# Kernel optimization log

Hardware: AMD Instinct MI355X
Metric: run time of the kernel (lower is better)

## Reference

```python
import jax, jax.numpy as jnp
import numpy as np

B, C, H, W = 8, 2, 512, 512  # features hard-coded to 2 by Conv3x3(2,1)
N_ATTN = 6  # 3 ResidualAttentionUnits x 2 AttentionConv each
HALF = C // 2


def _conv1x1(x, w, b):
    # x: [B,C,H,W], w: [O,C], b: [O]
    return jnp.einsum('bchw,oc->bohw', x, w) + b[None, :, None, None]


def _unfold3(x):
    # x: [B,C,H+2,W+2] -> [B,C,H,W,3,3] (height-window, width-window), matching
    # torch unfold(2,3,1).unfold(3,3,1)
    Hh = x.shape[2] - 2
    Ww = x.shape[3] - 2
    return jnp.stack(
        [jnp.stack([x[:, :, i:i + Hh, j:j + Ww] for j in range(3)], axis=-1)
         for i in range(3)], axis=-2)


def _attn_conv(x, wq, bq, wk, bk, wv, bv, rh, rw):
    # Local 3x3 window self-attention (AttentionConv, groups=1).
    b_, c_, h_, w_ = x.shape
    xp = jnp.pad(x, ((0, 0), (0, 0), (1, 1), (1, 1)))  # zero pad=1
    q = _conv1x1(x, wq, bq)                 # [B,Co,H,W]
    k = _unfold3(_conv1x1(xp, wk, bk))      # [B,Co,H,W,3,3]
    v = _unfold3(_conv1x1(xp, wv, bv))
    co = q.shape[1]
    half = co // 2
    # rh, rw: [half,3]; rel_h broadcast over kh, rel_w over kw
    k = jnp.concatenate([
        k[:, :half] + rh[None, :, None, None, :, None],
        k[:, half:] + rw[None, :, None, None, None, :]], axis=1)
    k = k.reshape(b_, co, h_, w_, 9)
    v = v.reshape(b_, co, h_, w_, 9)
    attn = jax.nn.softmax(q[..., None] * k, axis=-1)  # softmax over 9 window positions
    return jnp.einsum('bchwk,bchwk->bchw', attn, v)


def _rau(x, p, u):
    # ResidualAttentionUnit: relu -> atten1 -> relu -> atten2 -> +x
    wq, bq, wk, bk, wv, bv, rh, rw = p
    i, j = 2 * u, 2 * u + 1
    h = jax.nn.relu(x)
    h = _attn_conv(h, wq[i], bq[i], wk[i], bk[i], wv[i], bv[i], rh[i], rw[i])
    h = jax.nn.relu(h)
    h = _attn_conv(h, wq[j], bq[j], wk[j], bk[j], wv[j], bv[j], rh[j], rw[j])
    return h + x


def _up2_bilinear_ac(x):
    # bilinear, scale_factor=2, align_corners=True
    b_, c_, h_, w_ = x.shape
    ho, wo = 2 * h_, 2 * w_
    ys = jnp.linspace(0.0, h_ - 1.0, ho)
    xs = jnp.linspace(0.0, w_ - 1.0, wo)
    y0 = jnp.floor(ys).astype(jnp.int32)
    x0 = jnp.floor(xs).astype(jnp.int32)
    y1 = jnp.clip(y0 + 1, 0, h_ - 1)
    x1 = jnp.clip(x0 + 1, 0, w_ - 1)
    wy = (ys - y0)[None, None, :, None]
    wx = (xs - x0)[None, None, None, :]
    r0 = x[:, :, y0, :]
    r1 = x[:, :, y1, :]
    v00 = r0[:, :, :, x0]
    v01 = r0[:, :, :, x1]
    v10 = r1[:, :, :, x0]
    v11 = r1[:, :, :, x1]
    return (v00 * (1 - wy) * (1 - wx) + v01 * (1 - wy) * wx
            + v10 * wy * (1 - wx) + v11 * wy * wx)


def _forward(input_1, input_2, wq, bq, wk, bk, wv, bv, rh, rw, conv_w, conv_b):
    p = (wq, bq, wk, bk, wv, bv, rh, rw)
    out = _rau(input_1, p, 0) + _rau(input_2, p, 1)
    out = _rau(out, p, 2)
    xp = jnp.pad(out, ((0, 0), (0, 0), (1, 1), (1, 1)), mode='reflect')
    out = jax.lax.conv_general_dilated(
        xp, conv_w, (1, 1), 'VALID',
        dimension_numbers=('NCHW', 'OIHW', 'NCHW')) + conv_b[None, :, None, None]
    out = jax.nn.sigmoid(out)
    return out, _up2_bilinear_ac(out)


def setup_inputs() -> dict:
    key = jax.random.key(0)
    ks = jax.random.split(key, 12)
    return {
        'input_1': jax.random.normal(ks[0], (B, C, H, W), jnp.float32),
        'input_2': jax.random.normal(ks[1], (B, C, H, W), jnp.float32),
        # stacked params for the 6 AttentionConv modules (all bias=True)
        'wq': jax.random.normal(ks[2], (N_ATTN, C, C), jnp.float32) * 0.5,
        'bq': jax.random.normal(ks[3], (N_ATTN, C), jnp.float32) * 0.1,
        'wk': jax.random.normal(ks[4], (N_ATTN, C, C), jnp.float32) * 0.5,
        'bk': jax.random.normal(ks[5], (N_ATTN, C), jnp.float32) * 0.1,
        'wv': jax.random.normal(ks[6], (N_ATTN, C, C), jnp.float32) * 0.5,
        'bv': jax.random.normal(ks[7], (N_ATTN, C), jnp.float32) * 0.1,
        'rh': jax.random.normal(ks[8], (N_ATTN, HALF, 3), jnp.float32),
        'rw': jax.random.normal(ks[9], (N_ATTN, HALF, 3), jnp.float32),
        # Conv3x3(2,1): reflection-pad + 3x3 conv
        'conv_w': jax.random.normal(ks[10], (1, 2, 3, 3), jnp.float32) * 0.2,
        'conv_b': jax.random.normal(ks[11], (1,), jnp.float32) * 0.1,
    }


def reference(input_1, input_2, wq, bq, wk, bk, wv, bv, rh, rw, conv_w, conv_b):
    return _forward(input_1, input_2, wq, bq, wk, bk, wv, bv, rh, rw, conv_w, conv_b)
```

## Files before the change

### kernel.cpp

```cpp
#include <hip/hip_runtime.h>

#if __has_builtin(__builtin_amdgcn_exp2f)
#define EXP2F(x) __builtin_amdgcn_exp2f(x)
#else
#define EXP2F(x) exp2f(x)
#endif

typedef float v2f __attribute__((ext_vector_type(2)));

constexpr int B = 8, H = 512, W = 512;
constexpr int PLANE = H * W;
constexpr int BSTRIDE = 2 * PLANE;
constexpr int NPIX = B * PLANE;
constexpr int UPN = B * 1024 * 1024;
constexpr int PPITCH = 520;
constexpr int PXOFF  = 4;
constexpr int PPLANE = H * PPITCH;
constexpr int PBUF   = 16 * PPLANE;
constexpr float LOG2E = 1.4426950408889634f;

__device__ __forceinline__ float reluf(float v) { return v > 0.f ? v : 0.f; }
__device__ __forceinline__ float frcp(float v) { return __builtin_amdgcn_rcpf(v); }
__device__ __forceinline__ v2f vfma(v2f a, v2f b, v2f c) { return __builtin_elementwise_fma(a, b, c); }
__device__ __forceinline__ v2f vmax2(v2f a, v2f b) { return __builtin_elementwise_max(a, b); }
__device__ __forceinline__ v2f bc(float x) { v2f r; r.x = x; r.y = x; return r; }

struct AttnW {
    v2f wq0, wq1, bq;
    v2f wk0, wk1;
    v2f biasK[3];
    float rwL[3];
    v2f wv0, wv1, bv;
};

__device__ __forceinline__ AttnW load_w(
    const float* wq, const float* bq, const float* wk, const float* bk,
    const float* wv, const float* bv, const float* rh, const float* rw, int i)
{
    AttnW P;
    P.wq0.x = wq[4*i];   P.wq0.y = wq[4*i+2];
    P.wq1.x = wq[4*i+1]; P.wq1.y = wq[4*i+3];
    P.bq.x  = bq[2*i];   P.bq.y  = bq[2*i+1];
    P.wk0.x = wk[4*i]   * LOG2E; P.wk0.y = wk[4*i+2] * LOG2E;
    P.wk1.x = wk[4*i+1] * LOG2E; P.wk1.y = wk[4*i+3] * LOG2E;
    float bk1L = bk[2*i+1] * LOG2E;
#pragma unroll
    for (int r = 0; r < 3; ++r) {
        P.biasK[r].x = (bk[2*i] + rh[3*i+r]) * LOG2E;
        P.biasK[r].y = bk1L;
    }
#pragma unroll
    for (int d = 0; d < 3; ++d) P.rwL[d] = rw[3*i+d] * LOG2E;
    P.wv0.x = wv[4*i];   P.wv0.y = wv[4*i+2];
    P.wv1.x = wv[4*i+1]; P.wv1.y = wv[4*i+3];
    P.bv.x  = bv[2*i];   P.bv.y  = bv[2*i+1];
    return P;
}

__device__ __forceinline__ void attn_strip(
    const v2f (&t)[3][6], const AttnW& P, v2f (&o)[4])
{
    v2f kk[3][6], vv[3][6];
#pragma unroll
    for (int r = 0; r < 3; ++r)
#pragma unroll
        for (int c = 0; c < 6; ++c) {
            v2f u0 = bc(t[r][c].x), u1 = bc(t[r][c].y);
            kk[r][c] = vfma(P.wk0, u0, vfma(P.wk1, u1, P.biasK[r]));
            vv[r][c] = vfma(P.wv0, u0, vfma(P.wv1, u1, P.bv));
        }
#pragma unroll
    for (int px = 0; px < 4; ++px) {
        v2f q = vfma(P.wq0, bc(t[1][px+1].x), vfma(P.wq1, bc(t[1][px+1].y), P.bq));
        v2f addv[3];
#pragma unroll
        for (int d = 0; d < 3; ++d) { addv[d].x = 0.f; addv[d].y = q.y * P.rwL[d]; }
        v2f s[9];
#pragma unroll
        for (int r = 0; r < 3; ++r)
#pragma unroll
            for (int d = 0; d < 3; ++d)
                s[r*3+d] = vfma(q, kk[r][px+d], addv[d]);
        v2f m = vmax2(vmax2(vmax2(vmax2(s[0], s[1]), vmax2(s[2], s[3])),
                            vmax2(vmax2(s[4], s[5]), vmax2(s[6], s[7]))), s[8]);
        v2f sum = bc(0.f), acc = bc(0.f);
#pragma unroll
        for (int r = 0; r < 3; ++r)
#pragma unroll
            for (int d = 0; d < 3; ++d) {
                v2f dd = s[r*3+d] - m;
                v2f e; e.x = EXP2F(dd.x); e.y = EXP2F(dd.y);
                sum += e;
                acc = vfma(e, vv[r][px+d], acc);
            }
        v2f rs; rs.x = frcp(sum.x); rs.y = frcp(sum.y);
        o[px] = acc * rs;
    }
}

__device__ __forceinline__ void write_pads(float* outp, int b2, int y, int x0)
{
    float4 z = make_float4(0.f, 0.f, 0.f, 0.f);
    if (x0 == 0) {
        int pb = b2 * PPLANE + y * PPITCH;
        *reinterpret_cast<float4*>(outp + pb)          = z;
        *reinterpret_cast<float4*>(outp + pb + PPLANE) = z;
    } else if (x0 == W - 4) {
        int pb = b2 * PPLANE + y * PPITCH + PXOFF + W;
        *reinterpret_cast<float4*>(outp + pb)          = z;
        *reinterpret_cast<float4*>(outp + pb + PPLANE) = z;
    }
}

__global__ __launch_bounds__(256) void attn_in_kernel(
    const float* __restrict__ xA, const float* __restrict__ xB,
    float* __restrict__ outA, float* __restrict__ outB,
    const float* __restrict__ wq, const float* __restrict__ bq,
    const float* __restrict__ wk, const float* __restrict__ bk,
    const float* __restrict__ wv, const float* __restrict__ bv,
    const float* __restrict__ rh, const float* __restrict__ rw,
    int piA, int piB)
{
    int bid = blockIdx.x;
    bool second = bid >= 2048;
    const float* x = second ? xB : xA;
    float* outp = second ? outB : outA;
    int pi = second ? piB : piA;

    int s  = (second ? bid - 2048 : bid) * 256 + threadIdx.x;
    int x0 = (s & 127) * 4;
    int y  = (s >> 7) & 511;
    int b  = s >> 16;

    AttnW P = load_w(wq, bq, wk, bk, wv, bv, rh, rw, pi);

    const float* xb = x + b * BSTRIDE;
    bool rowv[3] = { y > 0, true, y < H - 1 };
    int  yr[3]   = { y > 0 ? y - 1 : 0, y, y < H - 1 ? y + 1 : H - 1 };
    bool lv   = x0 > 0;
    bool rvld = x0 < W - 4;
    int  xl = lv ? x0 - 1 : 0;
    int  xr = rvld ? x0 + 4 : W - 1;

    v2f t[3][6];
#pragma unroll
    for (int r = 0; r < 3; ++r) {
        const float* p0 = xb + yr[r] * W;
        const float* p1 = p0 + PLANE;
        float4 a0 = *reinterpret_cast<const float4*>(p0 + x0);
        float4 a1 = *reinterpret_cast<const float4*>(p1 + x0);
        float u0[6] = { p0[xl], a0.x, a0.y, a0.z, a0.w, p0[xr] };
        float u1[6] = { p1[xl], a1.x, a1.y, a1.z, a1.w, p1[xr] };
        bool rv_ = rowv[r];
#pragma unroll
        for (int c = 0; c < 6; ++c) {
            bool ok = rv_ && (c > 0 || lv) && (c < 5 || rvld);
            t[r][c].x = ok ? reluf(u0[c]) : 0.f;
            t[r][c].y = ok ? reluf(u1[c]) : 0.f;
        }
    }

    v2f o[4];
    attn_strip(t, P, o);

    int ob = (b * 2) * PPLANE + y * PPITCH + x0 + PXOFF;
    *reinterpret_cast<float4*>(outp + ob)          = make_float4(o[0].x, o[1].x, o[2].x, o[3].x);
    *reinterpret_cast<float4*>(outp + ob + PPLANE) = make_float4(o[0].y, o[1].y, o[2].y, o[3].y);
    write_pads(outp, b * 2, y, x0);
}

template<int NRES, bool PADOUT>
__global__ __launch_bounds__(256) void attn_fast_kernel(
    const float* __restrict__ xp,
    float* __restrict__ outp, int oPlane, int oPitch, int oXoff,
    const float* __restrict__ res0, int aPlane, int aPitch, int aXoff,
    const float* __restrict__ res1, int cPlane, int cPitch, int cXoff,
    const float* __restrict__ wq, const float* __restrict__ bq,
    const float* __restrict__ wk, const float* __restrict__ bk,
    const float* __restrict__ wv, const float* __restrict__ bv,
    const float* __restrict__ rh, const float* __restrict__ rw, int pi)
{
    int s  = blockIdx.x * 256 + threadIdx.x;
    int x0 = (s & 127) * 4;
    int y  = (s >> 7) & 511;
    int b  = s >> 16;

    AttnW P = load_w(wq, bq, wk, bk, wv, bv, rh, rw, pi);

    const float* xb0 = xp + (b * 2) * PPLANE + x0 + PXOFF;
    v2f t[3][6];
#pragma unroll
    for (int r = 0; r < 3; ++r) {
        int gy = y - 1 + r;
        bool ok = (unsigned)gy < (unsigned)H;
        int gyc = ok ? gy : y;
        const float* p0 = xb0 + gyc * PPITCH;
        const float* p1 = p0 + PPLANE;
        float4 a0 = *reinterpret_cast<const float4*>(p0);
        float4 a1 = *reinterpret_cast<const float4*>(p1);
        float e0l = p0[-1], e0r = p0[4];
        float e1l = p1[-1], e1r = p1[4];
        if (ok) {
            t[r][0].x=reluf(e0l);  t[r][0].y=reluf(e1l);
            t[r][1].x=reluf(a0.x); t[r][1].y=reluf(a1.x);
            t[r][2].x=reluf(a0.y); t[r][2].y=reluf(a1.y);
            t[r][3].x=reluf(a0.z); t[r][3].y=reluf(a1.z);
            t[r][4].x=reluf(a0.w); t[r][4].y=reluf(a1.w);
            t[r][5].x=reluf(e0r);  t[r][5].y=reluf(e1r);
        } else {
#pragma unroll
            for (int c = 0; c < 6; ++c) { t[r][c].x = 0.f; t[r][c].y = 0.f; }
        }
    }

    v2f o[4];
    attn_strip(t, P, o);

    if (NRES >= 1) {
        int rb = (b * 2) * aPlane + y * aPitch + x0 + aXoff;
        float4 ra = *reinterpret_cast<const float4*>(res0 + rb);
        float4 rbv = *reinterpret_cast<const float4*>(res0 + rb + aPlane);
        o[0].x+=ra.x; o[1].x+=ra.y; o[2].x+=ra.z; o[3].x+=ra.w;
        o[0].y+=rbv.x; o[1].y+=rbv.y; o[2].y+=rbv.z; o[3].y+=rbv.w;
    }
    if (NRES >= 2) {
        int rb = (b * 2) * cPlane + y * cPitch + x0 + cXoff;
        float4 ra = *reinterpret_cast<const float4*>(res1 + rb);
        float4 rbv = *reinterpret_cast<const float4*>(res1 + rb + cPlane);
        o[0].x+=ra.x; o[1].x+=ra.y; o[2].x+=ra.z; o[3].x+=ra.w;
        o[0].y+=rbv.x; o[1].y+=rbv.y; o[2].y+=rbv.z; o[3].y+=rbv.w;
    }

    int ob = (b * 2) * oPlane + y * oPitch + x0 + oXoff;
    *reinterpret_cast<float4*>(outp + ob)          = make_float4(o[0].x, o[1].x, o[2].x, o[3].x);
    *reinterpret_cast<float4*>(outp + ob + oPlane) = make_float4(o[0].y, o[1].y, o[2].y, o[3].y);
    if (PADOUT) write_pads(outp, b * 2, y, x0);
}

__global__ __launch_bounds__(256) void conv_sig4_kernel(
    const float* __restrict__ u,
    const float* __restrict__ cw, const float* __restrict__ cb,
    float* __restrict__ o)
{
    int s  = blockIdx.x * 256 + threadIdx.x;
    int x0 = (s & 127) * 4;
    int y  = (s >> 7) & 511;
    int b  = s >> 16;

    float w[18];
#pragma unroll
    for (int i = 0; i < 18; ++i) w[i] = cw[i];

    int yy[3];
#pragma unroll
    for (int i = 0; i < 3; ++i) {
        int t = y + i - 1;
        if (t < 0) t = -t;
        if (t > H - 1) t = 2 * (H - 1) - t;
        yy[i] = t;
    }
    int xl = x0 - 1; if (xl < 0) xl = 1;
    int xr = x0 + 4; if (xr > W - 1) xr = 2 * (W - 1) - xr;

    float acc[4] = { cb[0], cb[0], cb[0], cb[0] };
#pragma unroll
    for (int c = 0; c < 2; ++c) {
        const float* up = u + b * BSTRIDE + c * PLANE;
#pragma unroll
        for (int i = 0; i < 3; ++i) {
            const float* row = up + yy[i] * W;
            float4 a = *reinterpret_cast<const float4*>(row + x0);
            float t[6] = { row[xl], a.x, a.y, a.z, a.w, row[xr] };
#pragma unroll
            for (int j = 0; j < 3; ++j) {
                float wc = w[c * 9 + i * 3 + j];
#pragma unroll
                for (int px = 0; px < 4; ++px)
                    acc[px] = fmaf(t[px + j], wc, acc[px]);
            }
        }
    }
    float4 ov;
    ov.x = frcp(1.f + EXP2F(-acc[0] * LOG2E));
    ov.y = frcp(1.f + EXP2F(-acc[1] * LOG2E));
    ov.z = frcp(1.f + EXP2F(-acc[2] * LOG2E));
    ov.w = frcp(1.f + EXP2F(-acc[3] * LOG2E));
    *reinterpret_cast<float4*>(o + b * PLANE + y * W + x0) = ov;
}

__global__ __launch_bounds__(256) void upsample4_kernel(
    const float* __restrict__ o, float* __restrict__ up)
{
    int p  = blockIdx.x * 256 + threadIdx.x;
    int b  = p >> 18;
    int y  = (p >> 8) & 1023;
    int x0 = (p & 255) * 4;

    const float scale = 511.0f / 1023.0f;
    float fy = y * scale;
    int y0 = (int)fy;
    float wy = fy - y0;
    int y1 = min(y0 + 1, H - 1);

    const float* ob = o + b * PLANE;
    const float* row0 = ob + y0 * W;
    const float* row1 = ob + y1 * W;

    float4 ov;
    float* ovp = &ov.x;
#pragma unroll
    for (int j = 0; j < 4; ++j) {
        float fx = (x0 + j) * scale;
        int xi = (int)fx;
        float wx = fx - xi;
        int xi1 = min(xi + 1, W - 1);
        float v00 = row0[xi], v01 = row0[xi1];
        float v10 = row1[xi], v11 = row1[xi1];
        float top = fmaf(v01 - v00, wx, v00);
        float bot = fmaf(v11 - v10, wx, v10);
        ovp[j] = fmaf(bot - top, wy, top);
    }
    *reinterpret_cast<float4*>(up + ((long)b << 20) + y * 1024 + x0) = ov;
}

extern "C" void kernel_launch(void* const* d_in, const int* in_sizes, int n_in,
                              void* d_out, int out_size, void* d_ws, size_t ws_size,
                              hipStream_t stream) {
    const float* in1 = (const float*)d_in[0];
    const float* in2 = (const float*)d_in[1];
    const float* wq  = (const float*)d_in[2];
    const float* bq  = (const float*)d_in[3];
    const float* wk  = (const float*)d_in[4];
    const float* bk  = (const float*)d_in[5];
    const float* wv  = (const float*)d_in[6];
    const float* bv  = (const float*)d_in[7];
    const float* rh  = (const float*)d_in[8];
    const float* rw  = (const float*)d_in[9];
    const float* cw  = (const float*)d_in[10];
    const float* cb  = (const float*)d_in[11];

    float* out = (float*)d_out;
    float* A  = out;
    float* Bb = out + PBUF;
    float* C  = (float*)d_ws;
    (void)ws_size; (void)out_size; (void)n_in; (void)in_sizes;

    dim3 blk(256);

    attn_in_kernel<<<4096, blk, 0, stream>>>(in1, in2, A, Bb,
        wq, bq, wk, bk, wv, bv, rh, rw, 0, 2);
    attn_fast_kernel<1,false><<<2048, blk, 0, stream>>>(A, C, PLANE, W, 0,
        in1, PLANE, W, 0, nullptr, 0, 0, 0,
        wq, bq, wk, bk, wv, bv, rh, rw, 1);
    attn_fast_kernel<2,true><<<2048, blk, 0, stream>>>(Bb, A, PPLANE, PPITCH, PXOFF,
        in2, PLANE, W, 0, C, PLANE, W, 0,
        wq, bq, wk, bk, wv, bv, rh, rw, 3);
    attn_fast_kernel<0,true><<<2048, blk, 0, stream>>>(A, Bb, PPLANE, PPITCH, PXOFF,
        nullptr, 0, 0, 0, nullptr, 0, 0, 0,
        wq, bq, wk, bk, wv, bv, rh, rw, 4);
    attn_fast_kernel<1,false><<<2048, blk, 0, stream>>>(Bb, C, PLANE, W, 0,
        A, PPLANE, PPITCH, PXOFF, nullptr, 0, 0, 0,
        wq, bq, wk, bk, wv, bv, rh, rw, 5);
    conv_sig4_kernel<<<2048, blk, 0, stream>>>(C, cw, cb, out);
    upsample4_kernel<<<8192, blk, 0, stream>>>(out, out + NPIX);
}
```

Baseline: 115.7 us.

## Fuse all stages into one cooperative persistent kernel with grid barriers

```diff
diff --git a/kernel.cpp b/kernel.cpp
--- a/kernel.cpp
+++ b/kernel.cpp
@@ -12,7 +12,6 @@
 constexpr int PLANE = H * W;
 constexpr int BSTRIDE = 2 * PLANE;
 constexpr int NPIX = B * PLANE;
-constexpr int UPN = B * 1024 * 1024;
 constexpr int PPITCH = 520;
 constexpr int PXOFF  = 4;
 constexpr int PPLANE = H * PPITCH;
@@ -112,27 +111,13 @@
     }
 }
 
-__global__ __launch_bounds__(256) void attn_in_kernel(
-    const float* __restrict__ xA, const float* __restrict__ xB,
-    float* __restrict__ outA, float* __restrict__ outB,
-    const float* __restrict__ wq, const float* __restrict__ bq,
-    const float* __restrict__ wk, const float* __restrict__ bk,
-    const float* __restrict__ wv, const float* __restrict__ bv,
-    const float* __restrict__ rh, const float* __restrict__ rw,
-    int piA, int piB)
-{
-    int bid = blockIdx.x;
-    bool second = bid >= 2048;
-    const float* x = second ? xB : xA;
-    float* outp = second ? outB : outA;
-    int pi = second ? piB : piA;
-
-    int s  = (second ? bid - 2048 : bid) * 256 + threadIdx.x;
+
+__device__ __forceinline__ void attn_in_body(
+    unsigned s, const float* __restrict__ x, float* outp, const AttnW& P)
+{
     int x0 = (s & 127) * 4;
     int y  = (s >> 7) & 511;
     int b  = s >> 16;
-
-    AttnW P = load_w(wq, bq, wk, bk, wv, bv, rh, rw, pi);
 
     const float* xb = x + b * BSTRIDE;
     bool rowv[3] = { y > 0, true, y < H - 1 };
@@ -170,22 +155,16 @@
 }
 
 template<int NRES, bool PADOUT>
-__global__ __launch_bounds__(256) void attn_fast_kernel(
-    const float* __restrict__ xp,
-    float* __restrict__ outp, int oPlane, int oPitch, int oXoff,
-    const float* __restrict__ res0, int aPlane, int aPitch, int aXoff,
-    const float* __restrict__ res1, int cPlane, int cPitch, int cXoff,
-    const float* __restrict__ wq, const float* __restrict__ bq,
-    const float* __restrict__ wk, const float* __restrict__ bk,
-    const float* __restrict__ wv, const float* __restrict__ bv,
-    const float* __restrict__ rh, const float* __restrict__ rw, int pi)
-{
-    int s  = blockIdx.x * 256 + threadIdx.x;
+__device__ __forceinline__ void attn_fast_body(
+    unsigned s, const float* xp, float* outp,
+    int oPlane, int oPitch, int oXoff,
+    const float* res0, int aPlane, int aPitch, int aXoff,
+    const float* res1, int cPlane, int cPitch, int cXoff,
+    const AttnW& P)
+{
     int x0 = (s & 127) * 4;
     int y  = (s >> 7) & 511;
     int b  = s >> 16;
-
-    AttnW P = load_w(wq, bq, wk, bk, wv, bv, rh, rw, pi);
 
     const float* xb0 = xp + (b * 2) * PPLANE + x0 + PXOFF;
     v2f t[3][6];
@@ -237,19 +216,12 @@
     if (PADOUT) write_pads(outp, b * 2, y, x0);
 }
 
-__global__ __launch_bounds__(256) void conv_sig4_kernel(
-    const float* __restrict__ u,
-    const float* __restrict__ cw, const float* __restrict__ cb,
-    float* __restrict__ o)
-{
-    int s  = blockIdx.x * 256 + threadIdx.x;
+__device__ __forceinline__ void conv_body(
+    unsigned s, const float* u, const float (&w)[18], float cb0, float* o)
+{
     int x0 = (s & 127) * 4;
     int y  = (s >> 7) & 511;
     int b  = s >> 16;
-
-    float w[18];
-#pragma unroll
-    for (int i = 0; i < 18; ++i) w[i] = cw[i];
 
     int yy[3];
 #pragma unroll
@@ -262,7 +234,7 @@
     int xl = x0 - 1; if (xl < 0) xl = 1;
     int xr = x0 + 4; if (xr > W - 1) xr = 2 * (W - 1) - xr;
 
-    float acc[4] = { cb[0], cb[0], cb[0], cb[0] };
+    float acc[4] = { cb0, cb0, cb0, cb0 };
 #pragma unroll
     for (int c = 0; c < 2; ++c) {
         const float* up = u + b * BSTRIDE + c * PLANE;
@@ -288,10 +260,8 @@
     *reinterpret_cast<float4*>(o + b * PLANE + y * W + x0) = ov;
 }
 
-__global__ __launch_bounds__(256) void upsample4_kernel(
-    const float* __restrict__ o, float* __restrict__ up)
-{
-    int p  = blockIdx.x * 256 + threadIdx.x;
+__device__ __forceinline__ void up_body(unsigned p, const float* o, float* up)
+{
     int b  = p >> 18;
     int y  = (p >> 8) & 1023;
     int x0 = (p & 255) * 4;
@@ -321,6 +291,163 @@
         ovp[j] = fmaf(bot - top, wy, top);
     }
     *reinterpret_cast<float4*>(up + ((long)b << 20) + y * 1024 + x0) = ov;
+}
+
+__device__ __forceinline__ void grid_barrier(unsigned* bar, unsigned nblocks)
+{
+    __syncthreads();
+    if (threadIdx.x == 0) {
+        __threadfence();
+        unsigned g = __hip_atomic_load(&bar[1], __ATOMIC_RELAXED, __HIP_MEMORY_SCOPE_AGENT);
+        unsigned arrived = __hip_atomic_fetch_add(&bar[0], 1u, __ATOMIC_ACQ_REL, __HIP_MEMORY_SCOPE_AGENT);
+        if (arrived == nblocks - 1) {
+            __hip_atomic_store(&bar[0], 0u, __ATOMIC_RELAXED, __HIP_MEMORY_SCOPE_AGENT);
+            __hip_atomic_fetch_add(&bar[1], 1u, __ATOMIC_ACQ_REL, __HIP_MEMORY_SCOPE_AGENT);
+        } else {
+            while (__hip_atomic_load(&bar[1], __ATOMIC_ACQUIRE, __HIP_MEMORY_SCOPE_AGENT) == g)
+                __builtin_amdgcn_s_sleep(1);
+        }
+        __threadfence();
+    }
+    __syncthreads();
+}
+
+__device__ __forceinline__ void myrange(unsigned total, unsigned& w0, unsigned& w1)
+{
+    unsigned g = gridDim.x;
+    w0 = (total * blockIdx.x) / g;
+    w1 = (total * (blockIdx.x + 1)) / g;
+}
+
+__global__ __launch_bounds__(256) void mega_kernel(
+    const float* __restrict__ in1, const float* __restrict__ in2,
+    float* A, float* Bb, float* C, float* out,
+    const float* __restrict__ wq, const float* __restrict__ bq,
+    const float* __restrict__ wk, const float* __restrict__ bk,
+    const float* __restrict__ wv, const float* __restrict__ bv,
+    const float* __restrict__ rh, const float* __restrict__ rw,
+    const float* __restrict__ cw, const float* __restrict__ cb,
+    unsigned* bar)
+{
+    const unsigned nb = gridDim.x;
+    const unsigned tid = threadIdx.x;
+    unsigned w0, w1;
+
+    myrange(4096, w0, w1);
+    {
+        unsigned mid = w1 < 2048 ? w1 : 2048;
+        if (w0 < mid) {
+            AttnW PA = load_w(wq, bq, wk, bk, wv, bv, rh, rw, 0);
+            for (unsigned wb = w0; wb < mid; ++wb)
+                attn_in_body((wb << 8) | tid, in1, A, PA);
+        }
+        unsigned lo = w0 > 2048 ? w0 : 2048;
+        if (lo < w1) {
+            AttnW PB = load_w(wq, bq, wk, bk, wv, bv, rh, rw, 2);
+            for (unsigned wb = lo; wb < w1; ++wb)
+                attn_in_body(((wb - 2048) << 8) | tid, in2, Bb, PB);
+        }
+    }
+    grid_barrier(bar, nb);
+
+    myrange(2048, w0, w1);
+    {
+        AttnW P = load_w(wq, bq, wk, bk, wv, bv, rh, rw, 1);
+        for (unsigned wb = w0; wb < w1; ++wb)
+            attn_fast_body<1,false>((wb << 8) | tid, A, C, PLANE, W, 0,
+                in1, PLANE, W, 0, nullptr, 0, 0, 0, P);
+    }
+    grid_barrier(bar, nb);
+
+    myrange(2048, w0, w1);
+    {
+        AttnW P = load_w(wq, bq, wk, bk, wv, bv, rh, rw, 3);
+        for (unsigned wb = w0; wb < w1; ++wb)
+            attn_fast_body<2,true>((wb << 8) | tid, Bb, A, PPLANE, PPITCH, PXOFF,
+                in2, PLANE, W, 0, C, PLANE, W, 0, P);
+    }
+    grid_barrier(bar, nb);
+
+    myrange(2048, w0, w1);
+    {
+        AttnW P = load_w(wq, bq, wk, bk, wv, bv, rh, rw, 4);
+        for (unsigned wb = w0; wb < w1; ++wb)
+            attn_fast_body<0,true>((wb << 8) | tid, A, Bb, PPLANE, PPITCH, PXOFF,
+                nullptr, 0, 0, 0, nullptr, 0, 0, 0, P);
+    }
+    grid_barrier(bar, nb);
+
+    myrange(2048, w0, w1);
+    {
+        AttnW P = load_w(wq, bq, wk, bk, wv, bv, rh, rw, 5);
+        for (unsigned wb = w0; wb < w1; ++wb)
+            attn_fast_body<1,false>((wb << 8) | tid, Bb, C, PLANE, W, 0,
+                A, PPLANE, PPITCH, PXOFF, nullptr, 0, 0, 0, P);
+    }
+    grid_barrier(bar, nb);
+
+    myrange(2048, w0, w1);
+    {
+        float w18[18];
+#pragma unroll
+        for (int i = 0; i < 18; ++i) w18[i] = cw[i];
+        float cb0 = cb[0];
+        for (unsigned wb = w0; wb < w1; ++wb)
+            conv_body((wb << 8) | tid, C, w18, cb0, out);
+    }
+    grid_barrier(bar, nb);
+
+    myrange(8192, w0, w1);
+    for (unsigned wb = w0; wb < w1; ++wb)
+        up_body((wb << 8) | tid, out, out + NPIX);
+}
+
+
+__global__ __launch_bounds__(256) void attn_in_kernel(
+    const float* __restrict__ xA, const float* __restrict__ xB,
+    float* outA, float* outB,
+    const float* __restrict__ wq, const float* __restrict__ bq,
+    const float* __restrict__ wk, const float* __restrict__ bk,
+    const float* __restrict__ wv, const float* __restrict__ bv,
+    const float* __restrict__ rh, const float* __restrict__ rw,
+    int piA, int piB)
+{
+    int bid = blockIdx.x;
+    bool second = bid >= 2048;
+    AttnW P = load_w(wq, bq, wk, bk, wv, bv, rh, rw, second ? piB : piA);
+    unsigned s = (unsigned)(second ? bid - 2048 : bid) * 256u + threadIdx.x;
+    attn_in_body(s, second ? xB : xA, second ? outB : outA, P);
+}
+
+template<int NRES, bool PADOUT>
+__global__ __launch_bounds__(256) void attn_fast_kernel(
+    const float* xp, float* outp, int oPlane, int oPitch, int oXoff,
+    const float* res0, int aPlane, int aPitch, int aXoff,
+    const float* res1, int cPlane, int cPitch, int cXoff,
+    const float* __restrict__ wq, const float* __restrict__ bq,
+    const float* __restrict__ wk, const float* __restrict__ bk,
+    const float* __restrict__ wv, const float* __restrict__ bv,
+    const float* __restrict__ rh, const float* __restrict__ rw, int pi)
+{
+    AttnW P = load_w(wq, bq, wk, bk, wv, bv, rh, rw, pi);
+    unsigned s = blockIdx.x * 256u + threadIdx.x;
+    attn_fast_body<NRES,PADOUT>(s, xp, outp, oPlane, oPitch, oXoff,
+        res0, aPlane, aPitch, aXoff, res1, cPlane, cPitch, cXoff, P);
+}
+
+__global__ __launch_bounds__(256) void conv_sig4_kernel(
+    const float* u, const float* __restrict__ cw, const float* __restrict__ cb,
+    float* o)
+{
+    float w18[18];
+#pragma unroll
+    for (int i = 0; i < 18; ++i) w18[i] = cw[i];
+    conv_body(blockIdx.x * 256u + threadIdx.x, u, w18, cb[0], o);
+}
+
+__global__ __launch_bounds__(256) void upsample4_kernel(const float* o, float* up)
+{
+    up_body(blockIdx.x * 256u + threadIdx.x, o, up);
 }
 
 extern "C" void kernel_launch(void* const* d_in, const int* in_sizes, int n_in,
@@ -343,10 +470,35 @@
     float* A  = out;
     float* Bb = out + PBUF;
     float* C  = (float*)d_ws;
+    unsigned* bar = (unsigned*)(out + (2 * PBUF) + 64);
     (void)ws_size; (void)out_size; (void)n_in; (void)in_sizes;
 
+    int nbq = 0;
+    hipError_t qe = hipOccupancyMaxActiveBlocksPerMultiprocessor(
+        &nbq, reinterpret_cast<const void*>(mega_kernel), 256, 0);
+    if (qe == hipSuccess && nbq > 0) {
+        unsigned grid = (unsigned)nbq * 256u;
+        if (grid > 2048u) grid = 2048u;
+        hipMemsetAsync(bar, 0, 2 * sizeof(unsigned), stream);
+        const float *a_in1 = in1, *a_in2 = in2;
+        float *a_A = A, *a_B = Bb, *a_C = C, *a_out = out;
+        const float *a_wq = wq, *a_bq = bq, *a_wk = wk, *a_bk = bk;
+        const float *a_wv = wv, *a_bv = bv, *a_rh = rh, *a_rw = rw;
+        const float *a_cw = cw, *a_cb = cb;
+        unsigned* a_bar = bar;
+        void* args[] = {
+            (void*)&a_in1, (void*)&a_in2, (void*)&a_A, (void*)&a_B,
+            (void*)&a_C, (void*)&a_out,
+            (void*)&a_wq, (void*)&a_bq, (void*)&a_wk, (void*)&a_bk,
+            (void*)&a_wv, (void*)&a_bv, (void*)&a_rh, (void*)&a_rw,
+            (void*)&a_cw, (void*)&a_cb, (void*)&a_bar };
+        hipError_t le = hipLaunchCooperativeKernel(
+            reinterpret_cast<const void*>(mega_kernel),
+            dim3(grid), dim3(256), args, 0, stream);
+        if (le == hipSuccess) return;
+    }
+
     dim3 blk(256);
-
     attn_in_kernel<<<4096, blk, 0, stream>>>(in1, in2, A, Bb,
         wq, bq, wk, bk, wv, bv, rh, rw, 0, 2);
     attn_fast_kernel<1,false><<<2048, blk, 0, stream>>>(A, C, PLANE, W, 0,
```

Result: slower. 391.7 us (+238.4%).

## Fuse second-stage attention convs and swizzle block order across XCDs

Applied to the files above, without the earlier changes.

```diff
diff --git a/kernel.cpp b/kernel.cpp
--- a/kernel.cpp
+++ b/kernel.cpp
@@ -12,7 +12,6 @@
 constexpr int PLANE = H * W;
 constexpr int BSTRIDE = 2 * PLANE;
 constexpr int NPIX = B * PLANE;
-constexpr int UPN = B * 1024 * 1024;
 constexpr int PPITCH = 520;
 constexpr int PXOFF  = 4;
 constexpr int PPLANE = H * PPITCH;
@@ -24,6 +23,11 @@
 __device__ __forceinline__ v2f vfma(v2f a, v2f b, v2f c) { return __builtin_elementwise_fma(a, b, c); }
 __device__ __forceinline__ v2f vmax2(v2f a, v2f b) { return __builtin_elementwise_max(a, b); }
 __device__ __forceinline__ v2f bc(float x) { v2f r; r.x = x; r.y = x; return r; }
+
+__device__ __forceinline__ unsigned swz8(unsigned bid, unsigned nwg)
+{
+    return (bid & 7u) * (nwg >> 3) + (bid >> 3);
+}
 
 struct AttnW {
     v2f wq0, wq1, bq;
@@ -112,27 +116,13 @@
     }
 }
 
-__global__ __launch_bounds__(256) void attn_in_kernel(
-    const float* __restrict__ xA, const float* __restrict__ xB,
-    float* __restrict__ outA, float* __restrict__ outB,
-    const float* __restrict__ wq, const float* __restrict__ bq,
-    const float* __restrict__ wk, const float* __restrict__ bk,
-    const float* __restrict__ wv, const float* __restrict__ bv,
-    const float* __restrict__ rh, const float* __restrict__ rw,
-    int piA, int piB)
-{
-    int bid = blockIdx.x;
-    bool second = bid >= 2048;
-    const float* x = second ? xB : xA;
-    float* outp = second ? outB : outA;
-    int pi = second ? piB : piA;
-
-    int s  = (second ? bid - 2048 : bid) * 256 + threadIdx.x;
-    int x0 = (s & 127) * 4;
-    int y  = (s >> 7) & 511;
-    int b  = s >> 16;
-
-    AttnW P = load_w(wq, bq, wk, bk, wv, bv, rh, rw, pi);
+
+__device__ __forceinline__ void load_t_unpadded(
+    unsigned s, const float* __restrict__ x, v2f (&t)[3][6])
+{
+    int x0 = (s & 127) * 4;
+    int y  = (s >> 7) & 511;
+    int b  = s >> 16;
 
     const float* xb = x + b * BSTRIDE;
     bool rowv[3] = { y > 0, true, y < H - 1 };
@@ -142,7 +132,6 @@
     int  xl = lv ? x0 - 1 : 0;
     int  xr = rvld ? x0 + 4 : W - 1;
 
-    v2f t[3][6];
 #pragma unroll
     for (int r = 0; r < 3; ++r) {
         const float* p0 = xb + yr[r] * W;
@@ -159,36 +148,16 @@
             t[r][c].y = ok ? reluf(u1[c]) : 0.f;
         }
     }
-
-    v2f o[4];
-    attn_strip(t, P, o);
-
-    int ob = (b * 2) * PPLANE + y * PPITCH + x0 + PXOFF;
-    *reinterpret_cast<float4*>(outp + ob)          = make_float4(o[0].x, o[1].x, o[2].x, o[3].x);
-    *reinterpret_cast<float4*>(outp + ob + PPLANE) = make_float4(o[0].y, o[1].y, o[2].y, o[3].y);
-    write_pads(outp, b * 2, y, x0);
-}
-
-template<int NRES, bool PADOUT>
-__global__ __launch_bounds__(256) void attn_fast_kernel(
-    const float* __restrict__ xp,
-    float* __restrict__ outp, int oPlane, int oPitch, int oXoff,
-    const float* __restrict__ res0, int aPlane, int aPitch, int aXoff,
-    const float* __restrict__ res1, int cPlane, int cPitch, int cXoff,
-    const float* __restrict__ wq, const float* __restrict__ bq,
-    const float* __restrict__ wk, const float* __restrict__ bk,
-    const float* __restrict__ wv, const float* __restrict__ bv,
-    const float* __restrict__ rh, const float* __restrict__ rw, int pi)
-{
-    int s  = blockIdx.x * 256 + threadIdx.x;
-    int x0 = (s & 127) * 4;
-    int y  = (s >> 7) & 511;
-    int b  = s >> 16;
-
-    AttnW P = load_w(wq, bq, wk, bk, wv, bv, rh, rw, pi);
+}
+
+__device__ __forceinline__ void load_t_padded(
+    unsigned s, const float* __restrict__ xp, v2f (&t)[3][6])
+{
+    int x0 = (s & 127) * 4;
+    int y  = (s >> 7) & 511;
+    int b  = s >> 16;
 
     const float* xb0 = xp + (b * 2) * PPLANE + x0 + PXOFF;
-    v2f t[3][6];
 #pragma unroll
     for (int r = 0; r < 3; ++r) {
         int gy = y - 1 + r;
@@ -212,29 +181,130 @@
             for (int c = 0; c < 6; ++c) { t[r][c].x = 0.f; t[r][c].y = 0.f; }
         }
     }
-
+}
+
+
+__global__ __launch_bounds__(256) void attn_in_kernel(
+    const float* __restrict__ xA, const float* __restrict__ xB,
+    float* outA, float* outB,
+    const float* __restrict__ wq, const float* __restrict__ bq,
+    const float* __restrict__ wk, const float* __restrict__ bk,
+    const float* __restrict__ wv, const float* __restrict__ bv,
+    const float* __restrict__ rh, const float* __restrict__ rw,
+    int piA, int piB)
+{
+    unsigned wid = swz8(blockIdx.x, 4096);
+    bool second = wid >= 2048;
+    AttnW P = load_w(wq, bq, wk, bk, wv, bv, rh, rw, second ? piB : piA);
+    unsigned s = (second ? wid - 2048 : wid) * 256u + threadIdx.x;
+
+    v2f t[3][6];
+    load_t_unpadded(s, second ? xB : xA, t);
     v2f o[4];
     attn_strip(t, P, o);
 
-    if (NRES >= 1) {
-        int rb = (b * 2) * aPlane + y * aPitch + x0 + aXoff;
-        float4 ra = *reinterpret_cast<const float4*>(res0 + rb);
-        float4 rbv = *reinterpret_cast<const float4*>(res0 + rb + aPlane);
-        o[0].x+=ra.x; o[1].x+=ra.y; o[2].x+=ra.z; o[3].x+=ra.w;
-        o[0].y+=rbv.x; o[1].y+=rbv.y; o[2].y+=rbv.z; o[3].y+=rbv.w;
-    }
-    if (NRES >= 2) {
-        int rb = (b * 2) * cPlane + y * cPitch + x0 + cXoff;
-        float4 ra = *reinterpret_cast<const float4*>(res1 + rb);
-        float4 rbv = *reinterpret_cast<const float4*>(res1 + rb + cPlane);
-        o[0].x+=ra.x; o[1].x+=ra.y; o[2].x+=ra.z; o[3].x+=ra.w;
-        o[0].y+=rbv.x; o[1].y+=rbv.y; o[2].y+=rbv.z; o[3].y+=rbv.w;
-    }
-
-    int ob = (b * 2) * oPlane + y * oPitch + x0 + oXoff;
+    int x0 = (s & 127) * 4;
+    int y  = (s >> 7) & 511;
+    int b  = s >> 16;
+    float* outp = second ? outB : outA;
+    int ob = (b * 2) * PPLANE + y * PPITCH + x0 + PXOFF;
     *reinterpret_cast<float4*>(outp + ob)          = make_float4(o[0].x, o[1].x, o[2].x, o[3].x);
-    *reinterpret_cast<float4*>(outp + ob + oPlane) = make_float4(o[0].y, o[1].y, o[2].y, o[3].y);
-    if (PADOUT) write_pads(outp, b * 2, y, x0);
+    *reinterpret_cast<float4*>(outp + ob + PPLANE) = make_float4(o[0].y, o[1].y, o[2].y, o[3].y);
+    write_pads(outp, b * 2, y, x0);
+}
+
+__global__ __launch_bounds__(256) void attn_fused23_kernel(
+    const float* __restrict__ A, const float* __restrict__ Bb,
+    const float* __restrict__ in1, const float* __restrict__ in2,
+    float* __restrict__ C,
+    const float* __restrict__ wq, const float* __restrict__ bq,
+    const float* __restrict__ wk, const float* __restrict__ bk,
+    const float* __restrict__ wv, const float* __restrict__ bv,
+    const float* __restrict__ rh, const float* __restrict__ rw)
+{
+    unsigned s = swz8(blockIdx.x, 2048) * 256u + threadIdx.x;
+    int x0 = (s & 127) * 4;
+    int y  = (s >> 7) & 511;
+    int b  = s >> 16;
+    int base0 = b * BSTRIDE + y * W + x0;
+    int base1 = base0 + PLANE;
+
+    v2f t[3][6];
+    v2f o1[4], o2[4];
+
+    {
+        AttnW P1 = load_w(wq, bq, wk, bk, wv, bv, rh, rw, 1);
+        load_t_padded(s, A, t);
+        attn_strip(t, P1, o1);
+        float4 ra = *reinterpret_cast<const float4*>(in1 + base0);
+        float4 rb = *reinterpret_cast<const float4*>(in1 + base1);
+        o1[0].x += ra.x; o1[1].x += ra.y; o1[2].x += ra.z; o1[3].x += ra.w;
+        o1[0].y += rb.x; o1[1].y += rb.y; o1[2].y += rb.z; o1[3].y += rb.w;
+    }
+    {
+        AttnW P3 = load_w(wq, bq, wk, bk, wv, bv, rh, rw, 3);
+        load_t_padded(s, Bb, t);
+        attn_strip(t, P3, o2);
+        float4 ra = *reinterpret_cast<const float4*>(in2 + base0);
+        float4 rb = *reinterpret_cast<const float4*>(in2 + base1);
+        o2[0].x += ra.x + o1[0].x; o2[1].x += ra.y + o1[1].x;
+        o2[2].x += ra.z + o1[2].x; o2[3].x += ra.w + o1[3].x;
+        o2[0].y += rb.x + o1[0].y; o2[1].y += rb.y + o1[1].y;
+        o2[2].y += rb.z + o1[2].y; o2[3].y += rb.w + o1[3].y;
+    }
+
+    *reinterpret_cast<float4*>(C + base0) = make_float4(o2[0].x, o2[1].x, o2[2].x, o2[3].x);
+    *reinterpret_cast<float4*>(C + base1) = make_float4(o2[0].y, o2[1].y, o2[2].y, o2[3].y);
+}
+
+__global__ __launch_bounds__(256) void attn4_kernel(
+    const float* __restrict__ C, float* __restrict__ Bb,
+    const float* __restrict__ wq, const float* __restrict__ bq,
+    const float* __restrict__ wk, const float* __restrict__ bk,
+    const float* __restrict__ wv, const float* __restrict__ bv,
+    const float* __restrict__ rh, const float* __restrict__ rw)
+{
+    unsigned s = swz8(blockIdx.x, 2048) * 256u + threadIdx.x;
+    AttnW P = load_w(wq, bq, wk, bk, wv, bv, rh, rw, 4);
+    v2f t[3][6];
+    load_t_unpadded(s, C, t);
+    v2f o[4];
+    attn_strip(t, P, o);
+
+    int x0 = (s & 127) * 4;
+    int y  = (s >> 7) & 511;
+    int b  = s >> 16;
+    int ob = (b * 2) * PPLANE + y * PPITCH + x0 + PXOFF;
+    *reinterpret_cast<float4*>(Bb + ob)          = make_float4(o[0].x, o[1].x, o[2].x, o[3].x);
+    *reinterpret_cast<float4*>(Bb + ob + PPLANE) = make_float4(o[0].y, o[1].y, o[2].y, o[3].y);
+    write_pads(Bb, b * 2, y, x0);
+}
+
+__global__ __launch_bounds__(256) void attn5_kernel(
+    const float* __restrict__ Bb, float* __restrict__ C,
+    const float* __restrict__ wq, const float* __restrict__ bq,
+    const float* __restrict__ wk, const float* __restrict__ bk,
+    const float* __restrict__ wv, const float* __restrict__ bv,
+    const float* __restrict__ rh, const float* __restrict__ rw)
+{
+    unsigned s = swz8(blockIdx.x, 2048) * 256u + threadIdx.x;
+    AttnW P = load_w(wq, bq, wk, bk, wv, bv, rh, rw, 5);
+    v2f t[3][6];
+    load_t_padded(s, Bb, t);
+    v2f o[4];
+    attn_strip(t, P, o);
+
+    int x0 = (s & 127) * 4;
+    int y  = (s >> 7) & 511;
+    int b  = s >> 16;
+    int base0 = b * BSTRIDE + y * W + x0;
+    int base1 = base0 + PLANE;
+    float4 ra = *reinterpret_cast<const float4*>(C + base0);
+    float4 rb = *reinterpret_cast<const float4*>(C + base1);
+    o[0].x += ra.x; o[1].x += ra.y; o[2].x += ra.z; o[3].x += ra.w;
+    o[0].y += rb.x; o[1].y += rb.y; o[2].y += rb.z; o[3].y += rb.w;
+    *reinterpret_cast<float4*>(C + base0) = make_float4(o[0].x, o[1].x, o[2].x, o[3].x);
+    *reinterpret_cast<float4*>(C + base1) = make_float4(o[0].y, o[1].y, o[2].y, o[3].y);
 }
 
 __global__ __launch_bounds__(256) void conv_sig4_kernel(
@@ -242,7 +312,7 @@
     const float* __restrict__ cw, const float* __restrict__ cb,
     float* __restrict__ o)
 {
-    int s  = blockIdx.x * 256 + threadIdx.x;
+    unsigned s = swz8(blockIdx.x, 2048) * 256u + threadIdx.x;
     int x0 = (s & 127) * 4;
     int y  = (s >> 7) & 511;
     int b  = s >> 16;
@@ -291,7 +361,7 @@
 __global__ __launch_bounds__(256) void upsample4_kernel(
     const float* __restrict__ o, float* __restrict__ up)
 {
-    int p  = blockIdx.x * 256 + threadIdx.x;
+    unsigned p = swz8(blockIdx.x, 8192) * 256u + threadIdx.x;
     int b  = p >> 18;
     int y  = (p >> 8) & 1023;
     int x0 = (p & 255) * 4;
@@ -349,18 +419,12 @@
 
     attn_in_kernel<<<4096, blk, 0, stream>>>(in1, in2, A, Bb,
         wq, bq, wk, bk, wv, bv, rh, rw, 0, 2);
-    attn_fast_kernel<1,false><<<2048, blk, 0, stream>>>(A, C, PLANE, W, 0,
-        in1, PLANE, W, 0, nullptr, 0, 0, 0,
-        wq, bq, wk, bk, wv, bv, rh, rw, 1);
-    attn_fast_kernel<2,true><<<2048, blk, 0, stream>>>(Bb, A, PPLANE, PPITCH, PXOFF,
-        in2, PLANE, W, 0, C, PLANE, W, 0,
-        wq, bq, wk, bk, wv, bv, rh, rw, 3);
-    attn_fast_kernel<0,true><<<2048, blk, 0, stream>>>(A, Bb, PPLANE, PPITCH, PXOFF,
-        nullptr, 0, 0, 0, nullptr, 0, 0, 0,
-        wq, bq, wk, bk, wv, bv, rh, rw, 4);
-    attn_fast_kernel<1,false><<<2048, blk, 0, stream>>>(Bb, C, PLANE, W, 0,
-        A, PPLANE, PPITCH, PXOFF, nullptr, 0, 0, 0,
-        wq, bq, wk, bk, wv, bv, rh, rw, 5);
+    attn_fused23_kernel<<<2048, blk, 0, stream>>>(A, Bb, in1, in2, C,
+        wq, bq, wk, bk, wv, bv, rh, rw);
+    attn4_kernel<<<2048, blk, 0, stream>>>(C, Bb,
+        wq, bq, wk, bk, wv, bv, rh, rw);
+    attn5_kernel<<<2048, blk, 0, stream>>>(Bb, C,
+        wq, bq, wk, bk, wv, bv, rh, rw);
     conv_sig4_kernel<<<2048, blk, 0, stream>>>(C, cw, cb, out);
     upsample4_kernel<<<8192, blk, 0, stream>>>(out, out + NPIX);
 }
```

Result: faster. 105.2 us (-9.1%).
